# Performance work log

Measured on AMD Instinct MI355X. Metric: run time of the kernel, lower is better.

Reference implementation:

```python
import jax, jax.numpy as jnp
import numpy as np

N_NODES = 50000


def gcn_conv(x, W, b, src, dst, ew, n_nodes):
    """PyG GCNConv with edge weights: symmetric norm + self-loops (weight 1)."""
    h = x @ W  # [N, out]
    loop = jnp.arange(n_nodes, dtype=src.dtype)
    src2 = jnp.concatenate([src, loop])
    dst2 = jnp.concatenate([dst, loop])
    ew2 = jnp.concatenate([ew, jnp.ones((n_nodes,), dtype=ew.dtype)])
    deg = jax.ops.segment_sum(ew2, dst2, num_segments=n_nodes)  # [N]
    dinv = jnp.where(deg > 0, jax.lax.rsqrt(jnp.where(deg > 0, deg, 1.0)), 0.0)
    norm = dinv[src2] * ew2 * dinv[dst2]  # [E+N]
    msgs = h[src2] * norm[:, None]  # [E+N, out]
    out = jax.ops.segment_sum(msgs, dst2, num_segments=n_nodes)  # [N, out]
    return out + b


def setup_inputs() -> dict:
    key = jax.random.key(0)
    k = jax.random.split(key, 8)
    n, e = N_NODES, 800000
    c_in, c_hid, c_out = 256, 128, 128
    x = jax.random.normal(k[0], (n, c_in), dtype=jnp.float32)
    edge_index = jax.random.randint(k[1], (2, e), 0, n, dtype=jnp.int64)
    edge_attr = jax.random.uniform(k[2], (e,), dtype=jnp.float32)
    s1 = 1.0 / np.sqrt(c_in)
    s2 = 1.0 / np.sqrt(c_hid)
    W1 = jax.random.uniform(k[3], (c_in, c_hid), jnp.float32, -s1, s1)
    b1 = jnp.zeros((c_hid,), jnp.float32)
    W2 = jax.random.uniform(k[4], (c_hid, c_out), jnp.float32, -s2, s2)
    b2 = jnp.zeros((c_out,), jnp.float32)
    return {"x": x, "edge_index": edge_index, "edge_attr": edge_attr,
            "W1": W1, "b1": b1, "W2": W2, "b2": b2}


def reference(x, edge_index, edge_attr, W1, b1, W2, b2):
    src, dst = edge_index[0], edge_index[1]
    n = x.shape[0]
    h = jax.nn.relu(gcn_conv(x, W1, b1, src, dst, edge_attr, n))
    out = jax.nn.relu(gcn_conv(h, W2, b2, src, dst, edge_attr, n))
    return out
```

## Files before the change

kernel.cpp:

```cpp
#include <hip/hip_runtime.h>
#include <hip/hip_fp16.h>

#define COUT 128
#define SLOTS 48
#define BUCKCAP 5120

typedef unsigned char u8;
typedef unsigned short u16;
typedef unsigned int u32;
typedef unsigned long long u64;
typedef __attribute__((ext_vector_type(8))) short bf16x8;
typedef __attribute__((ext_vector_type(4))) float f32x4;

__device__ __forceinline__ u16 f2bf(float f) {
  u32 u = __builtin_bit_cast(u32, f);
  u += 0x7fffu + ((u >> 16) & 1u);
  return (u16)(u >> 16);
}
__device__ __forceinline__ float bf2f(u16 h) {
  u32 u = ((u32)h) << 16;
  return __builtin_bit_cast(float, u);
}
__device__ __forceinline__ float degf(u32 c) {
  return 1.0f + (float)(c & 0xFFFFFFu) * (1.0f / 262144.0f);
}

__global__ void init_kernel(u32* __restrict__ gbucket, int nbw,
                            const float* __restrict__ W1, u16* __restrict__ Wt1h, u16* __restrict__ Wt1l,
                            const float* __restrict__ W2, u16* __restrict__ Wt2h, u16* __restrict__ Wt2l,
                            int zb, int w1b) {
  int b = blockIdx.x;
  if (b < zb) {
    int i = b * 256 + threadIdx.x;
    if (i < nbw) gbucket[i] = 0u;
  } else if (b < zb + w1b) {
    int idx = (b - zb) * 256 + threadIdx.x;
    int nn = idx >> 8, kk = idx & 255;
    float v = W1[(size_t)kk * COUT + nn];
    u16 h = f2bf(v);
    Wt1h[idx] = h;
    Wt1l[idx] = f2bf(v - bf2f(h));
  } else {
    int idx = (b - zb - w1b) * 256 + threadIdx.x;
    int nn = idx >> 7, kk = idx & 127;
    float v = W2[(size_t)kk * COUT + nn];
    u16 h = f2bf(v);
    Wt2h[idx] = h;
    Wt2l[idx] = f2bf(v - bf2f(h));
  }
}

__global__ __launch_bounds__(256) void fused_g1pa_kernel(
    const float* __restrict__ A, const u16* __restrict__ Wth, const u16* __restrict__ Wtl,
    u16* __restrict__ H, int n,
    const int* __restrict__ src, const int* __restrict__ dst, const float* __restrict__ ew,
    u32* __restrict__ gbucket, u64* __restrict__ staging, int E, int crblk, int nbuck) {
  __shared__ u16 Ah[64 * 32], Al[64 * 32], Bh[128 * 32], Bl[128 * 32];
  __shared__ u32 bhist[256], bbase[256];
  const int g = blockIdx.x;
  const int tid = threadIdx.x;
  if (g & 1) {
    int half = g >> 1;
    if (half >= crblk) return;
    int e0 = half * 2048 + tid * 8;
    bool act = e0 < E;
    bhist[tid] = 0u;
    __syncthreads();
    int bk[8];
    u32 lr[8];
    u64 rec[8];
    if (act) {
      int4 d0 = *(const int4*)(dst + e0), d1 = *(const int4*)(dst + e0 + 4);
      int4 s0 = *(const int4*)(src + e0), s1 = *(const int4*)(src + e0 + 4);
      float4 w0 = *(const float4*)(ew + e0), w1 = *(const float4*)(ew + e0 + 4);
      int dd[8] = {d0.x, d0.y, d0.z, d0.w, d1.x, d1.y, d1.z, d1.w};
      int ss[8] = {s0.x, s0.y, s0.z, s0.w, s1.x, s1.y, s1.z, s1.w};
      float wwv[8] = {w0.x, w0.y, w0.z, w0.w, w1.x, w1.y, w1.z, w1.w};
#pragma unroll
      for (int j = 0; j < 8; ++j) {
        bk[j] = dd[j] >> 8;
        lr[j] = atomicAdd(&bhist[bk[j]], 1u);
        u64 lo = (u32)ss[j] | ((u32)(dd[j] & 255) << 16);
        u64 ewf = (u64)__half_as_ushort(__float2half(wwv[j]));
        u64 fix = (u64)(u32)__float2uint_rn(wwv[j] * 262144.0f);
        rec[j] = lo | (ewf << 24) | (fix << 40);
      }
    }
    __syncthreads();
    if (tid < nbuck && bhist[tid]) bbase[tid] = atomicAdd(&gbucket[tid * 16], bhist[tid]);
    __syncthreads();
    if (act) {
#pragma unroll
      for (int j = 0; j < 8; ++j) {
        u32 off = bbase[bk[j]] + lr[j];
        if (off < BUCKCAP) staging[(size_t)bk[j] * BUCKCAP + off] = rec[j];
      }
    }
    return;
  }
  const int row0 = (g >> 1) * 64;
  const int lane = tid & 63;
  const int w = tid >> 6;
  const int wr = w >> 1, wc = w & 1;
  const int r15 = lane & 15, q4 = lane >> 4;
  const int swz = q4 ^ ((r15 >> 1) & 3);

  f32x4 acc[2][4] = {};

  const int arow = tid >> 2, ac = tid & 3;
  const int sw_a = ac ^ ((arow >> 1) & 3);
  const bool arow_ok = (row0 + arow) < n;

  for (int k0 = 0; k0 < 256; k0 += 32) {
    if (k0) __syncthreads();
    float v[8];
    if (arow_ok) {
      const float* aptr = A + (size_t)(row0 + arow) * 256 + k0 + ac * 8;
      float4 p0 = *(const float4*)aptr;
      float4 p1 = *(const float4*)(aptr + 4);
      v[0] = p0.x; v[1] = p0.y; v[2] = p0.z; v[3] = p0.w;
      v[4] = p1.x; v[5] = p1.y; v[6] = p1.z; v[7] = p1.w;
    } else {
#pragma unroll
      for (int j = 0; j < 8; ++j) v[j] = 0.f;
    }
    bf16x8 hv, lv;
#pragma unroll
    for (int j = 0; j < 8; ++j) {
      u16 h = f2bf(v[j]);
      hv[j] = (short)h;
      lv[j] = (short)f2bf(v[j] - bf2f(h));
    }
    *(bf16x8*)&Ah[arow * 32 + sw_a * 8] = hv;
    *(bf16x8*)&Al[arow * 32 + sw_a * 8] = lv;
#pragma unroll
    for (int rep = 0; rep < 2; ++rep) {
      int q = tid + rep * 256;
      int nrow = q >> 2, cd = q & 3;
      int dstp = nrow * 32 + (cd ^ ((nrow >> 1) & 3)) * 8;
      *(bf16x8*)&Bh[dstp] = *(const bf16x8*)(Wth + (size_t)nrow * 256 + k0 + cd * 8);
      *(bf16x8*)&Bl[dstp] = *(const bf16x8*)(Wtl + (size_t)nrow * 256 + k0 + cd * 8);
    }
    __syncthreads();
    bf16x8 aH[2], aL[2], bH[4], bL[4];
#pragma unroll
    for (int mt = 0; mt < 2; ++mt) {
      int off = (wr * 32 + mt * 16 + r15) * 32 + swz * 8;
      aH[mt] = *(bf16x8*)&Ah[off];
      aL[mt] = *(bf16x8*)&Al[off];
    }
#pragma unroll
    for (int nt = 0; nt < 4; ++nt) {
      int off = (wc * 64 + nt * 16 + r15) * 32 + swz * 8;
      bH[nt] = *(bf16x8*)&Bh[off];
      bL[nt] = *(bf16x8*)&Bl[off];
    }
#pragma unroll
    for (int mt = 0; mt < 2; ++mt)
#pragma unroll
      for (int nt = 0; nt < 4; ++nt) {
        acc[mt][nt] = __builtin_amdgcn_mfma_f32_16x16x32_bf16(aH[mt], bH[nt], acc[mt][nt], 0, 0, 0);
        acc[mt][nt] = __builtin_amdgcn_mfma_f32_16x16x32_bf16(aH[mt], bL[nt], acc[mt][nt], 0, 0, 0);
        acc[mt][nt] = __builtin_amdgcn_mfma_f32_16x16x32_bf16(aL[mt], bH[nt], acc[mt][nt], 0, 0, 0);
      }
  }
#pragma unroll
  for (int mt = 0; mt < 2; ++mt) {
    int rbase = row0 + wr * 32 + mt * 16 + q4 * 4;
#pragma unroll
    for (int nt = 0; nt < 4; ++nt) {
      int col = wc * 64 + nt * 16 + r15;
#pragma unroll
      for (int j = 0; j < 4; ++j) {
        int r = rbase + j;
        if (r < n) H[(size_t)r * COUT + col] = f2bf(acc[mt][nt][j]);
      }
    }
  }
}

__global__ __launch_bounds__(256) void passB_kernel(const u64* __restrict__ staging,
                                                    const u32* __restrict__ gbucket,
                                                    u32* __restrict__ slots,
                                                    u32* __restrict__ cnt32,
                                                    float* __restrict__ dinv, int n) {
  __shared__ u32 packed[256];
  int b = blockIdx.x;
  int tid = threadIdx.x;
  packed[tid] = 0u;
  __syncthreads();
  int count = (int)gbucket[b * 16];
  if (count > BUCKCAP) count = BUCKCAP;
  const u64* srec = staging + (size_t)b * BUCKCAP;
  for (int base = 0; base < count; base += 256) {
    int idx = base + tid;
    if (idx < count) {
      u64 rec = srec[idx];
      u32 srcw = (u32)(rec & 0xFFFFu);
      u32 dlow = (u32)((rec >> 16) & 0xFFu);
      u32 ewf = (u32)((rec >> 24) & 0xFFFFu);
      u32 fix = (u32)((rec >> 40) & 0x7FFFFu);
      u32 old = atomicAdd(&packed[dlow], (1u << 24) | fix);
      u32 rank = old >> 24;
      if (rank < SLOTS) slots[((size_t)b * 256 + dlow) * SLOTS + rank] = srcw | (ewf << 16);
    }
  }
  __syncthreads();
  int node = b * 256 + tid;
  if (node < n) {
    u32 p = packed[tid];
    cnt32[node] = p;
    dinv[node] = rsqrtf(degf(p));
  }
}

__global__ __launch_bounds__(256) void gemm2_kernel(const u16* __restrict__ A,
                                                    const u16* __restrict__ Wth,
                                                    const u16* __restrict__ Wtl,
                                                    u16* __restrict__ H,
                                                    const float* __restrict__ dinv, int n) {
  __shared__ u16 Ah[64 * 32];
  __shared__ u16 Bh[128 * 32], Bl[128 * 32];
  const int tid = threadIdx.x;
  const int row0 = blockIdx.x * 64;
  const int lane = tid & 63;
  const int w = tid >> 6;
  const int wr = w >> 1, wc = w & 1;
  const int r15 = lane & 15, q4 = lane >> 4;
  const int swz = q4 ^ ((r15 >> 1) & 3);

  f32x4 acc[2][4] = {};

  const int arow = tid >> 2, ac = tid & 3;
  const int sw_a = ac ^ ((arow >> 1) & 3);
  const bool arow_ok = (row0 + arow) < n;

  for (int k0 = 0; k0 < 128; k0 += 32) {
    if (k0) __syncthreads();
    bf16x8 hv = {};
    if (arow_ok) hv = *(const bf16x8*)(A + (size_t)(row0 + arow) * 128 + k0 + ac * 8);
    *(bf16x8*)&Ah[arow * 32 + sw_a * 8] = hv;
#pragma unroll
    for (int rep = 0; rep < 2; ++rep) {
      int q = tid + rep * 256;
      int nrow = q >> 2, cd = q & 3;
      int dstp = nrow * 32 + (cd ^ ((nrow >> 1) & 3)) * 8;
      *(bf16x8*)&Bh[dstp] = *(const bf16x8*)(Wth + (size_t)nrow * 128 + k0 + cd * 8);
      *(bf16x8*)&Bl[dstp] = *(const bf16x8*)(Wtl + (size_t)nrow * 128 + k0 + cd * 8);
    }
    __syncthreads();
    bf16x8 aH[2], bH[4], bL[4];
#pragma unroll
    for (int mt = 0; mt < 2; ++mt)
      aH[mt] = *(bf16x8*)&Ah[(wr * 32 + mt * 16 + r15) * 32 + swz * 8];
#pragma unroll
    for (int nt = 0; nt < 4; ++nt) {
      int off = (wc * 64 + nt * 16 + r15) * 32 + swz * 8;
      bH[nt] = *(bf16x8*)&Bh[off];
      bL[nt] = *(bf16x8*)&Bl[off];
    }
#pragma unroll
    for (int mt = 0; mt < 2; ++mt)
#pragma unroll
      for (int nt = 0; nt < 4; ++nt) {
        acc[mt][nt] = __builtin_amdgcn_mfma_f32_16x16x32_bf16(aH[mt], bH[nt], acc[mt][nt], 0, 0, 0);
        acc[mt][nt] = __builtin_amdgcn_mfma_f32_16x16x32_bf16(aH[mt], bL[nt], acc[mt][nt], 0, 0, 0);
      }
  }
#pragma unroll
  for (int mt = 0; mt < 2; ++mt) {
    int rbase = row0 + wr * 32 + mt * 16 + q4 * 4;
#pragma unroll
    for (int nt = 0; nt < 4; ++nt) {
      int col = wc * 64 + nt * 16 + r15;
#pragma unroll
      for (int j = 0; j < 4; ++j) {
        int r = rbase + j;
        if (r < n) H[(size_t)r * COUT + col] = f2bf(dinv[r] * acc[mt][nt][j]);
      }
    }
  }
}

__device__ __forceinline__ void acc8(const uint4& hv, float w, float* acc) {
  u32 a0 = hv.x, a1 = hv.y, a2 = hv.z, a3 = hv.w;
  acc[0] += w * __builtin_bit_cast(float, a0 << 16);
  acc[1] += w * __builtin_bit_cast(float, a0 & 0xffff0000u);
  acc[2] += w * __builtin_bit_cast(float, a1 << 16);
  acc[3] += w * __builtin_bit_cast(float, a1 & 0xffff0000u);
  acc[4] += w * __builtin_bit_cast(float, a2 << 16);
  acc[5] += w * __builtin_bit_cast(float, a2 & 0xffff0000u);
  acc[6] += w * __builtin_bit_cast(float, a3 << 16);
  acc[7] += w * __builtin_bit_cast(float, a3 & 0xffff0000u);
}

template <bool SCALE_SRC, bool BF16_OUT>
__global__ __launch_bounds__(256) void agg_kernel(const uint4* __restrict__ h,
                                                  const float* __restrict__ dinv,
                                                  const u32* __restrict__ cnt32,
                                                  const u32* __restrict__ slots,
                                                  const float* __restrict__ bias,
                                                  void* __restrict__ outp, int n) {
  int node = blockIdx.x * 4 + (threadIdx.x >> 6);
  if (node >= n) return;
  int lane = threadIdx.x & 63;
  int g = lane >> 4, sub = lane & 15;
  float di = dinv[node];
  int cnt = (int)(cnt32[node] >> 24);
  if (cnt > SLOTS) cnt = SLOTS;
  float acc[8] = {};
  uint4 own = h[(size_t)node * 16 + sub];
  acc8(own, (g == 0) ? (SCALE_SRC ? di : 1.0f) : 0.f, acc);
  const u32* srow = slots + (size_t)node * SLOTS;
  for (int base = 0; base < cnt; base += 16) {
    u32 c[4];
    uint4 v[4];
    float w[4];
#pragma unroll
    for (int u = 0; u < 4; ++u) {
      int e = base + u * 4 + g;
      c[u] = (e < cnt) ? srow[e] : (u32)(node & 0xFFFF);
    }
#pragma unroll
    for (int u = 0; u < 4; ++u) {
      int s = (int)(c[u] & 0xFFFFu);
      v[u] = h[(size_t)s * 16 + sub];
      float ww = __half2float(__ushort_as_half((u16)(c[u] >> 16)));
      w[u] = SCALE_SRC ? ww * dinv[s] : ww;
    }
#pragma unroll
    for (int u = 0; u < 4; ++u) acc8(v[u], w[u], acc);
  }
#pragma unroll
  for (int j = 0; j < 8; ++j) {
    acc[j] += __shfl_xor(acc[j], 16);
    acc[j] += __shfl_xor(acc[j], 32);
  }
  int c0 = sub * 8 + g * 2;
  float2 bv = *(const float2*)(bias + c0);
  float r0 = fmaxf(acc[g * 2] * di + bv.x, 0.f);
  float r1 = fmaxf(acc[g * 2 + 1] * di + bv.y, 0.f);
  if constexpr (BF16_OUT) {
    ((u32*)outp)[(size_t)node * 64 + (c0 >> 1)] = (u32)f2bf(r0) | ((u32)f2bf(r1) << 16);
  } else {
    *(float2*)((float*)outp + (size_t)node * COUT + c0) = make_float2(r0, r1);
  }
}


extern "C" void kernel_launch(void* const* d_in, const int* in_sizes, int n_in,
                              void* d_out, int out_size, void* d_ws, size_t ws_size,
                              hipStream_t stream) {
  const float* x  = (const float*)d_in[0];
  const int*   ei = (const int*)d_in[1];
  const float* ew = (const float*)d_in[2];
  const float* W1 = (const float*)d_in[3];
  const float* b1 = (const float*)d_in[4];
  const float* W2 = (const float*)d_in[5];
  const float* b2 = (const float*)d_in[6];
  float* out = (float*)d_out;

  const int cin = 256;
  const int n = in_sizes[0] / cin;
  const int E = in_sizes[2];
  const int* srcp = ei;
  const int* dstp = ei + E;
  const int nbuck = (n + 255) >> 8;

  char* base = (char*)d_ws;
  size_t off = 0;
  auto alloc = [&](size_t bytes) -> void* {
    off = (off + 255) & ~(size_t)255;
    void* p = base + off;
    off += bytes;
    return p;
  };
  u32*   gbucket  = (u32*)alloc((size_t)nbuck * 16 * sizeof(u32));
  u64*   staging  = (u64*)alloc((size_t)nbuck * BUCKCAP * sizeof(u64));
  u32*   slots    = (u32*)alloc((size_t)n * SLOTS * sizeof(u32));
  u32*   cnt32    = (u32*)alloc((size_t)n * sizeof(u32));
  float* dinv     = (float*)alloc((size_t)n * sizeof(float));
  u16*   Wt1h     = (u16*)alloc((size_t)128 * 256 * sizeof(u16));
  u16*   Wt1l     = (u16*)alloc((size_t)128 * 256 * sizeof(u16));
  u16*   Wt2h     = (u16*)alloc((size_t)128 * 128 * sizeof(u16));
  u16*   Wt2l     = (u16*)alloc((size_t)128 * 128 * sizeof(u16));
  u16*   h16      = (u16*)alloc((size_t)n * COUT * sizeof(u16));
  u16*   o1b      = (u16*)alloc((size_t)n * COUT * sizeof(u16));

  const int tb = 256;
  const int zb = (nbuck * 16 + 255) / 256;
  const int w1b = 256 * COUT / 256;
  const int w2b = 128 * COUT / 256;
  const int gblk = (n + 63) / 64;
  const int ablk = (n + 3) / 4;
  const int crblk = (E + 2047) / 2048;
  const int fblk = 2 * ((gblk > crblk) ? gblk : crblk);

  init_kernel<<<zb + w1b + w2b, tb, 0, stream>>>(gbucket, nbuck * 16, W1, Wt1h, Wt1l, W2, Wt2h, Wt2l, zb, w1b);
  fused_g1pa_kernel<<<fblk, tb, 0, stream>>>(x, Wt1h, Wt1l, h16, n,
                                             srcp, dstp, ew, gbucket, staging, E, crblk, nbuck);
  passB_kernel<<<nbuck, tb, 0, stream>>>(staging, gbucket, slots, cnt32, dinv, n);

  agg_kernel<true, true><<<ablk, tb, 0, stream>>>((const uint4*)h16, dinv, cnt32, slots, b1, o1b, n);
  gemm2_kernel<<<gblk, tb, 0, stream>>>(o1b, Wt2h, Wt2l, h16, dinv, n);
  agg_kernel<false, false><<<ablk, tb, 0, stream>>>((const uint4*)h16, dinv, cnt32, slots, b2, out, n);
}
```

Baseline: 125.0 us.

## Locally sort edge records by bucket in LDS before coalesced staging writes

The edge-bucketing blocks now compute an exclusive scan of the per-block bucket histogram, scatter records into a shared-memory sorted buffer, and then write them to global staging in contiguous order. Each thread finds its record's bucket by binary search over the offsets. This replaces scattered 8-byte global stores with runs of consecutive addresses per bucket to improve write coalescing, at the cost of extra scans, barriers and LDS traffic. Shared memory is unified with the GEMM tiles via aliasing, which is why a barrier is added at the start of every k iteration.

```diff
diff --git a/kernel.cpp b/kernel.cpp
--- a/kernel.cpp
+++ b/kernel.cpp
@@ -55,31 +55,36 @@
     u16* __restrict__ H, int n,
     const int* __restrict__ src, const int* __restrict__ dst, const float* __restrict__ ew,
     u32* __restrict__ gbucket, u64* __restrict__ staging, int E, int crblk, int nbuck) {
-  __shared__ u16 Ah[64 * 32], Al[64 * 32], Bh[128 * 32], Bl[128 * 32];
-  __shared__ u32 bhist[256], bbase[256];
+  __shared__ u64 smem[3072];
+  __shared__ u32 wsum[8];
   const int g = blockIdx.x;
   const int tid = threadIdx.x;
   if (g & 1) {
     int half = g >> 1;
     if (half >= crblk) return;
-    int e0 = half * 2048 + tid * 8;
-    bool act = e0 < E;
-    bhist[tid] = 0u;
-    __syncthreads();
+    u64* sorted = smem;
+    u32* ofs    = (u32*)(smem + 2048);
+    u32* hist   = ofs + 260;
+    u32* bbase  = hist + 256;
+    int e0 = half * 2048;
+    hist[tid] = 0u;
+    __syncthreads();
+    int eb = e0 + tid * 8;
+    bool act = eb < E;
     int bk[8];
     u32 lr[8];
     u64 rec[8];
     if (act) {
-      int4 d0 = *(const int4*)(dst + e0), d1 = *(const int4*)(dst + e0 + 4);
-      int4 s0 = *(const int4*)(src + e0), s1 = *(const int4*)(src + e0 + 4);
-      float4 w0 = *(const float4*)(ew + e0), w1 = *(const float4*)(ew + e0 + 4);
+      int4 d0 = *(const int4*)(dst + eb), d1 = *(const int4*)(dst + eb + 4);
+      int4 s0 = *(const int4*)(src + eb), s1 = *(const int4*)(src + eb + 4);
+      float4 w0 = *(const float4*)(ew + eb), w1 = *(const float4*)(ew + eb + 4);
       int dd[8] = {d0.x, d0.y, d0.z, d0.w, d1.x, d1.y, d1.z, d1.w};
       int ss[8] = {s0.x, s0.y, s0.z, s0.w, s1.x, s1.y, s1.z, s1.w};
       float wwv[8] = {w0.x, w0.y, w0.z, w0.w, w1.x, w1.y, w1.z, w1.w};
 #pragma unroll
       for (int j = 0; j < 8; ++j) {
         bk[j] = dd[j] >> 8;
-        lr[j] = atomicAdd(&bhist[bk[j]], 1u);
+        lr[j] = atomicAdd(&hist[bk[j]], 1u);
         u64 lo = (u32)ss[j] | ((u32)(dd[j] & 255) << 16);
         u64 ewf = (u64)__half_as_ushort(__float2half(wwv[j]));
         u64 fix = (u64)(u32)__float2uint_rn(wwv[j] * 262144.0f);
@@ -87,17 +92,56 @@
       }
     }
     __syncthreads();
-    if (tid < nbuck && bhist[tid]) bbase[tid] = atomicAdd(&gbucket[tid * 16], bhist[tid]);
+    {
+      int lane = tid & 63, wid = tid >> 6;
+      u32 v = hist[tid];
+      u32 incl = v;
+#pragma unroll
+      for (int o = 1; o < 64; o <<= 1) {
+        u32 t = __shfl_up(incl, o);
+        if (lane >= o) incl += t;
+      }
+      if (lane == 63) wsum[wid] = incl;
+      __syncthreads();
+      if (tid < 4) {
+        u32 x = wsum[tid];
+#pragma unroll
+        for (int o = 1; o < 4; o <<= 1) {
+          u32 t = __shfl_up(x, o);
+          if (tid >= o) x += t;
+        }
+        wsum[tid + 4] = x;
+      }
+      __syncthreads();
+      u32 woff = (wid > 0) ? wsum[3 + wid] : 0u;
+      ofs[tid] = woff + incl - v;
+      if (tid == 255) ofs[256] = woff + incl;
+    }
+    if (tid < nbuck && hist[tid]) bbase[tid] = atomicAdd(&gbucket[tid * 16], hist[tid]);
     __syncthreads();
     if (act) {
 #pragma unroll
-      for (int j = 0; j < 8; ++j) {
-        u32 off = bbase[bk[j]] + lr[j];
-        if (off < BUCKCAP) staging[(size_t)bk[j] * BUCKCAP + off] = rec[j];
-      }
+      for (int j = 0; j < 8; ++j) sorted[ofs[bk[j]] + lr[j]] = rec[j];
+    }
+    __syncthreads();
+    int total = (int)ofs[256];
+    for (int i = tid; i < total; i += 256) {
+      int b = 0;
+#pragma unroll
+      for (int st = 128; st >= 1; st >>= 1) {
+        int nb = b + st;
+        if (nb < 256 && ofs[nb] <= (u32)i) b = nb;
+      }
+      u64 rc = sorted[i];
+      u32 pos = bbase[b] + (u32)i - ofs[b];
+      if (pos < BUCKCAP) staging[(size_t)b * BUCKCAP + pos] = rc;
     }
     return;
   }
+  u16* Ah = (u16*)smem;
+  u16* Al = Ah + 2048;
+  u16* Bh = Al + 2048;
+  u16* Bl = Bh + 4096;
   const int row0 = (g >> 1) * 64;
   const int lane = tid & 63;
   const int w = tid >> 6;
@@ -112,7 +156,7 @@
   const bool arow_ok = (row0 + arow) < n;
 
   for (int k0 = 0; k0 < 256; k0 += 32) {
-    if (k0) __syncthreads();
+    __syncthreads();
     float v[8];
     if (arow_ok) {
       const float* aptr = A + (size_t)(row0 + arow) * 256 + k0 + ac * 8;
```

Measured after the change: 125.6 us. Within noise of the previous version (+0.5%).
